# Kernel optimization log

Measured on AMD Instinct MI355X. Metric: run time of the kernel, lower is better.

## Reference

```python
import jax, jax.numpy as jnp
import numpy as np

N = 131072      # total nodes
E = 2097152     # total edges (~16 avg degree)
G = 1024        # number of graphs for mean pooling
NODE_DIM, EDGE_DIM, HID, OUT = 16, 6, 64, 128


def _lin(key, i, o):
    return jax.random.normal(key, (i, o), jnp.float32) * (1.0 / np.sqrt(i))


def setup_inputs() -> dict:
    key = jax.random.key(0)
    ks = jax.random.split(key, 12)
    return {
        "x": jax.random.normal(ks[0], (N, NODE_DIM), jnp.float32),
        "edge_attr": jax.random.normal(ks[1], (E, EDGE_DIM), jnp.float32),
        "edge_index": jax.random.randint(ks[2], (2, E), 0, N, jnp.int32),
        "batch": jnp.sort(jax.random.randint(ks[3], (N,), 0, G, jnp.int32)),
        # edge_mlp1: 2*16+6 -> 64 -> 64
        "w11": _lin(ks[4], 2 * NODE_DIM + EDGE_DIM, 64), "b11": jnp.zeros((64,), jnp.float32),
        "w12": _lin(ks[5], 64, HID), "b12": jnp.zeros((HID,), jnp.float32),
        # edge_mlp2: 2*64+6 -> 64 -> 64
        "w21": _lin(ks[6], 2 * HID + EDGE_DIM, 64), "b21": jnp.zeros((64,), jnp.float32),
        "w22": _lin(ks[7], 64, HID), "b22": jnp.zeros((HID,), jnp.float32),
        # readout: 64 -> 64 -> 128
        "wr1": _lin(ks[8], HID, 64), "br1": jnp.zeros((64,), jnp.float32),
        "wr2": _lin(ks[9], 64, OUT), "br2": jnp.zeros((OUT,), jnp.float32),
    }


def _edge_conv(h, edge_attr, src, dst, w1, b1, w2, b2):
    # PyG EdgeConv(aggr='max'): x_i = h[dst], x_j = h[src], scatter-max onto dst
    m = jnp.concatenate([h[dst], h[src], edge_attr], axis=-1)   # [E, 2D+edge_dim]
    m = jax.nn.relu(m @ w1 + b1) @ w2 + b2                       # [E, HID]
    agg = jax.ops.segment_max(m, dst, num_segments=h.shape[0])   # [N, HID]
    return jnp.where(jnp.isfinite(agg), agg, jnp.zeros_like(agg))  # empty nodes -> 0


def reference(x, edge_attr, edge_index, batch,
              w11, b11, w12, b12, w21, b21, w22, b22, wr1, br1, wr2, br2):
    src, dst = edge_index[0], edge_index[1]
    h = jax.nn.relu(_edge_conv(x, edge_attr, src, dst, w11, b11, w12, b12))
    h = jax.nn.relu(_edge_conv(h, edge_attr, src, dst, w21, b21, w22, b22))
    # global_mean_pool over batch ids
    sums = jax.ops.segment_sum(h, batch, num_segments=G)                       # [G, HID]
    cnts = jax.ops.segment_sum(jnp.ones((h.shape[0], 1), h.dtype), batch, num_segments=G)
    pooled = sums / jnp.maximum(cnts, 1.0)
    z = jax.nn.relu(pooled @ wr1 + br1) @ wr2 + br2                            # [G, OUT]
    return z
```

## Files before the change

### kernel.cpp

```cpp
#include <hip/hip_runtime.h>
#include <stdint.h>

#define NN 131072
#define NE 2097152
#define NG 1024

__device__ __forceinline__ unsigned enc_f32(float f) {
  unsigned b = __float_as_uint(f);
  return (b & 0x80000000u) ? ~b : (b | 0x80000000u);
}
__device__ __forceinline__ float dec_pos(unsigned u) {
  return __uint_as_float(u & 0x7fffffffu);
}

__global__ void init_ws(uint4* __restrict__ h1, uint4* __restrict__ h2,
                        int* __restrict__ counts, int* __restrict__ fill,
                        int* __restrict__ bcnt) {
  const int HN4 = NN * 64 / 4;
  uint4 v = make_uint4(0x80000000u, 0x80000000u, 0x80000000u, 0x80000000u);
  int stride = gridDim.x * blockDim.x;
  for (int t = blockIdx.x * blockDim.x + threadIdx.x; t < HN4; t += stride) {
    h1[t] = v;
    h2[t] = v;
  }
  for (int t = blockIdx.x * blockDim.x + threadIdx.x; t < NN; t += stride) {
    counts[t] = 0;
    fill[t] = 0;
  }
  for (int t = blockIdx.x * blockDim.x + threadIdx.x; t < NG; t += stride)
    bcnt[t] = 0;
}

__global__ __launch_bounds__(256) void count_all(const int* __restrict__ dst,
                                                 const int* __restrict__ batch,
                                                 int* __restrict__ counts,
                                                 int* __restrict__ bcnt) {
  int e = blockIdx.x * 256 + threadIdx.x;
  atomicAdd(&counts[dst[e]], 1);
  if (e < NN) atomicAdd(&bcnt[batch[e]], 1);
}

__global__ __launch_bounds__(256) void scanA(const int* __restrict__ counts,
                                             int* __restrict__ rp,
                                             int* __restrict__ bsum) {
  __shared__ int sm[256];
  int t = threadIdx.x;
  int g = blockIdx.x * 256 + t;
  int v = counts[g];
  sm[t] = v;
  __syncthreads();
  for (int off = 1; off < 256; off <<= 1) {
    int a = (t >= off) ? sm[t - off] : 0;
    __syncthreads();
    sm[t] += a;
    __syncthreads();
  }
  rp[g] = sm[t] - v;
  if (t == 255) bsum[blockIdx.x] = sm[255];
}

__global__ __launch_bounds__(512) void scanB(int* __restrict__ bsum) {
  __shared__ int sm[512];
  int t = threadIdx.x;
  int v = bsum[t];
  sm[t] = v;
  __syncthreads();
  for (int off = 1; off < 512; off <<= 1) {
    int a = (t >= off) ? sm[t - off] : 0;
    __syncthreads();
    sm[t] += a;
    __syncthreads();
  }
  bsum[t] = sm[t] - v;
}

__global__ __launch_bounds__(256) void scanC(int* __restrict__ rp,
                                             const int* __restrict__ bsum) {
  int g = blockIdx.x * 256 + threadIdx.x;
  rp[g] += bsum[blockIdx.x];
  if (g == 0) rp[NN] = NE;
}

__global__ __launch_bounds__(1024) void scan_batch(const int* __restrict__ bcnt,
                                                   int* __restrict__ bp) {
  __shared__ int sm[1024];
  int t = threadIdx.x;
  int v = bcnt[t];
  sm[t] = v;
  __syncthreads();
  for (int off = 1; off < 1024; off <<= 1) {
    int a = (t >= off) ? sm[t - off] : 0;
    __syncthreads();
    sm[t] += a;
    __syncthreads();
  }
  bp[t] = sm[t] - v;
  if (t == 1023) bp[NG] = NN;
}

__global__ __launch_bounds__(256) void scatter(
    const int* __restrict__ src, const int* __restrict__ dst,
    const float* __restrict__ ea, const int* __restrict__ rp,
    int* __restrict__ fill, int* __restrict__ eperm, int* __restrict__ sp,
    int* __restrict__ dst_p, float* __restrict__ ea_p, int use_eap) {
  int e = blockIdx.x * 256 + threadIdx.x;
  int d = dst[e];
  int p = rp[d] + atomicAdd(&fill[d], 1);
  sp[p] = src[e];
  dst_p[p] = d;
  if (use_eap) {
    const float2* s2 = (const float2*)(ea + (size_t)e * 6);
    float2 a = s2[0], b = s2[1], c = s2[2];
    float2* d2 = (float2*)(ea_p + (size_t)p * 6);
    d2[0] = a; d2[1] = b; d2[2] = c;
  } else {
    eperm[p] = e;
  }
}

__global__ __launch_bounds__(256, 4) void nodePQ1(
    const float* __restrict__ x, const float* __restrict__ w1,
    const float* __restrict__ b1, float* __restrict__ P, float* __restrict__ Q) {
  int half = blockIdx.x >> 9;
  int n = (blockIdx.x & 511) * 256 + threadIdx.x;
  const float* w = w1 + half * 16 * 64;
  float acc[64];
#pragma unroll
  for (int j = 0; j < 64; j++) acc[j] = half ? 0.0f : b1[j];
  const float4* x4 = (const float4*)(x + (size_t)n * 16);
#pragma unroll
  for (int kk = 0; kk < 4; kk++) {
    float4 v = x4[kk];
    const float* wr = w + (kk * 4) * 64;
#pragma unroll
    for (int j = 0; j < 64; j++) acc[j] = fmaf(v.x, wr[j], acc[j]);
#pragma unroll
    for (int j = 0; j < 64; j++) acc[j] = fmaf(v.y, wr[64 + j], acc[j]);
#pragma unroll
    for (int j = 0; j < 64; j++) acc[j] = fmaf(v.z, wr[128 + j], acc[j]);
#pragma unroll
    for (int j = 0; j < 64; j++) acc[j] = fmaf(v.w, wr[192 + j], acc[j]);
  }
  float4* o = (float4*)((half ? Q : P) + (size_t)n * 64);
#pragma unroll
  for (int j = 0; j < 16; j++)
    o[j] = make_float4(acc[4 * j], acc[4 * j + 1], acc[4 * j + 2], acc[4 * j + 3]);
}

__global__ __launch_bounds__(256, 4) void nodePQ2(
    const unsigned* __restrict__ h1, const float* __restrict__ w1,
    const float* __restrict__ b1, float* __restrict__ P, float* __restrict__ Q) {
  int half = blockIdx.x >> 9;
  int n = (blockIdx.x & 511) * 256 + threadIdx.x;
  const float* w = w1 + half * 64 * 64;
  float acc[64];
#pragma unroll
  for (int j = 0; j < 64; j++) acc[j] = half ? 0.0f : b1[j];
  const uint4* h4 = (const uint4*)(h1 + (size_t)n * 64);
#pragma unroll 4
  for (int kk = 0; kk < 16; kk++) {
    uint4 u = h4[kk];
    float v0 = dec_pos(u.x), v1 = dec_pos(u.y), v2 = dec_pos(u.z), v3 = dec_pos(u.w);
    const float* wr = w + (kk * 4) * 64;
#pragma unroll
    for (int j = 0; j < 64; j++) acc[j] = fmaf(v0, wr[j], acc[j]);
#pragma unroll
    for (int j = 0; j < 64; j++) acc[j] = fmaf(v1, wr[64 + j], acc[j]);
#pragma unroll
    for (int j = 0; j < 64; j++) acc[j] = fmaf(v2, wr[128 + j], acc[j]);
#pragma unroll
    for (int j = 0; j < 64; j++) acc[j] = fmaf(v3, wr[192 + j], acc[j]);
  }
  float4* o = (float4*)((half ? Q : P) + (size_t)n * 64);
#pragma unroll
  for (int j = 0; j < 16; j++)
    o[j] = make_float4(acc[4 * j], acc[4 * j + 1], acc[4 * j + 2], acc[4 * j + 3]);
}

template <bool EAP>
__global__ __launch_bounds__(256, 4) void edge_mlp(
    const float* __restrict__ P, const float* __restrict__ Q,
    const float* __restrict__ ea_p, const float* __restrict__ ea,
    const int* __restrict__ eperm, const int* __restrict__ sp,
    const int* __restrict__ dst_p, const int* __restrict__ rp,
    const float* __restrict__ w1c, const float* __restrict__ w2,
    const float* __restrict__ b2, unsigned* __restrict__ hout) {
  __shared__ float tile[4][64 * 32];
  __shared__ int dar[4][64];

  int tid = threadIdx.x;
  int wv = tid >> 6, lane = tid & 63;
  int g = blockIdx.x * 256 + tid;
  int wavebase = g - lane;
  int d = dst_p[g], s = sp[g];
  int seg_lo = rp[d], seg_hi = rp[d + 1];
  bool whole = (seg_lo >= wavebase) && (seg_hi <= wavebase + 64);
  dar[wv][lane] = d | (whole ? (int)0x80000000 : 0);

  float2 ev[3];
  if (EAP) {
    const float2* q = (const float2*)(ea_p + (size_t)g * 6);
    ev[0] = q[0]; ev[1] = q[1]; ev[2] = q[2];
  } else {
    int e = eperm[g];
    const float2* q = (const float2*)(ea + (size_t)e * 6);
    ev[0] = q[0]; ev[1] = q[1]; ev[2] = q[2];
  }

  const float4* Pd = (const float4*)(P + (size_t)d * 64);
  const float4* Qs = (const float4*)(Q + (size_t)s * 64);
  float* mytile = tile[wv];
  int swz = (lane & 7) << 2;

#pragma unroll 1
  for (int half = 0; half < 2; ++half) {
    float out[32];
#pragma unroll
    for (int o = 0; o < 32; o++) out[o] = b2[half * 32 + o];

#pragma unroll 1
    for (int jc = 0; jc < 4; ++jc) {
      float hj[16];
#pragma unroll
      for (int kk = 0; kk < 4; kk++) {
        float4 a = Pd[jc * 4 + kk];
        float4 b = Qs[jc * 4 + kk];
        hj[4 * kk]     = a.x + b.x;
        hj[4 * kk + 1] = a.y + b.y;
        hj[4 * kk + 2] = a.z + b.z;
        hj[4 * kk + 3] = a.w + b.w;
      }
#pragma unroll
      for (int t = 0; t < 3; t++) {
        const float* wr = w1c + (2 * t) * 64 + jc * 16;
#pragma unroll
        for (int j = 0; j < 16; j++) hj[j] = fmaf(ev[t].x, wr[j], hj[j]);
#pragma unroll
        for (int j = 0; j < 16; j++) hj[j] = fmaf(ev[t].y, wr[64 + j], hj[j]);
      }
#pragma unroll
      for (int j = 0; j < 16; j++) hj[j] = fmaxf(hj[j], 0.0f);

#pragma unroll
      for (int j = 0; j < 16; j++) {
        float hv = hj[j];
        const float* w2r = w2 + (jc * 16 + j) * 64 + half * 32;
#pragma unroll
        for (int o = 0; o < 32; o++) out[o] = fmaf(hv, w2r[o], out[o]);
      }
    }

#pragma unroll
    for (int k = 0; k < 8; ++k) {
      int cdst = (4 * k) ^ swz;
      *(float4*)&mytile[lane * 32 + cdst] =
          make_float4(out[4 * k], out[4 * k + 1], out[4 * k + 2], out[4 * k + 3]);
    }
    asm volatile("s_waitcnt lgkmcnt(0)" ::: "memory");

    if (lane < 32) {
      float mx = 0.0f;
      int cur = dar[wv][0];
#pragma unroll 8
      for (int e = 0; e < 64; ++e) {
        float v = mytile[e * 32 + (lane ^ ((e & 7) << 2))];
        mx = fmaxf(mx, v);
        int nxt = (e < 63) ? dar[wv][e + 1] : 0x7fffffff;
        if (cur != nxt) {
          unsigned encv = enc_f32(mx);
          unsigned* addr =
              hout + (size_t)(cur & 0x7fffffff) * 64 + half * 32 + lane;
          if (cur < 0) *addr = encv;
          else atomicMax(addr, encv);
          mx = 0.0f;
        }
        cur = nxt;
      }
    }
    asm volatile("s_waitcnt lgkmcnt(0)" ::: "memory");
  }
}

__global__ __launch_bounds__(256) void readout(
    const unsigned* __restrict__ h2, const int* __restrict__ bp,
    const float* __restrict__ wr1, const float* __restrict__ br1,
    const float* __restrict__ wr2, const float* __restrict__ br2,
    float* __restrict__ out) {
  int g = blockIdx.x;
  int tid = threadIdx.x;
  int wv = tid >> 6, lane = tid & 63;
  int lo = bp[g], hi = bp[g + 1];
  float s = 0.0f;
  for (int n = lo + wv; n < hi; n += 4) s += dec_pos(h2[(size_t)n * 64 + lane]);
  __shared__ float part[4][64];
  __shared__ float p[64], t[64];
  part[wv][lane] = s;
  __syncthreads();
  if (tid < 64) {
    float c = fmaxf((float)(hi - lo), 1.0f);
    p[tid] = (part[0][tid] + part[1][tid] + part[2][tid] + part[3][tid]) / c;
  }
  __syncthreads();
  if (tid < 64) {
    float a = br1[tid];
#pragma unroll 8
    for (int k = 0; k < 64; k++) a = fmaf(p[k], wr1[k * 64 + tid], a);
    t[tid] = fmaxf(a, 0.0f);
  }
  __syncthreads();
  if (tid < 64) {
    float z0 = br2[tid], z1 = br2[64 + tid];
#pragma unroll 8
    for (int k = 0; k < 64; k++) {
      float tk = t[k];
      z0 = fmaf(tk, wr2[k * 128 + tid], z0);
      z1 = fmaf(tk, wr2[k * 128 + 64 + tid], z1);
    }
    out[(size_t)g * 128 + tid] = z0;
    out[(size_t)g * 128 + 64 + tid] = z1;
  }
}

extern "C" void kernel_launch(void* const* d_in, const int* in_sizes, int n_in,
                              void* d_out, int out_size, void* d_ws, size_t ws_size,
                              hipStream_t stream) {
  const float* x     = (const float*)d_in[0];
  const float* ea    = (const float*)d_in[1];
  const int*   ei    = (const int*)d_in[2];
  const int*   batch = (const int*)d_in[3];
  const float* w11 = (const float*)d_in[4];
  const float* b11 = (const float*)d_in[5];
  const float* w12 = (const float*)d_in[6];
  const float* b12 = (const float*)d_in[7];
  const float* w21 = (const float*)d_in[8];
  const float* b21 = (const float*)d_in[9];
  const float* w22 = (const float*)d_in[10];
  const float* b22 = (const float*)d_in[11];
  const float* wr1 = (const float*)d_in[12];
  const float* br1 = (const float*)d_in[13];
  const float* wr2 = (const float*)d_in[14];
  const float* br2 = (const float*)d_in[15];
  float* out = (float*)d_out;

  const int* src = ei;
  const int* dst = ei + NE;

  char* ws = (char*)d_ws;
  size_t off = 0;
  auto alloc = [&](size_t bytes) {
    char* p = ws + off;
    off = (off + bytes + 255) & ~(size_t)255;
    return p;
  };
  unsigned* h1   = (unsigned*)alloc((size_t)NN * 64 * 4);
  unsigned* h2   = (unsigned*)alloc((size_t)NN * 64 * 4);
  float*    Pbuf = (float*)alloc((size_t)NN * 64 * 4);
  float*    Qbuf = (float*)alloc((size_t)NN * 64 * 4);
  int*   sp    = (int*)alloc((size_t)NE * 4);
  int*   eperm = (int*)alloc((size_t)NE * 4);
  int*   dst_p = (int*)alloc((size_t)NE * 4);
  int*   rp    = (int*)alloc((size_t)(NN + 1) * 4);
  int*   counts= (int*)alloc((size_t)NN * 4);
  int*   fill  = (int*)alloc((size_t)NN * 4);
  int*   bcnt  = (int*)alloc((size_t)NG * 4);
  int*   bp    = (int*)alloc((size_t)(NG + 1) * 4);
  int*   bsum  = (int*)alloc(512 * 4);
  float* ea_p  = (float*)alloc((size_t)NE * 6 * 4);
  int use_eap = (off <= ws_size) ? 1 : 0;

  init_ws<<<1024, 256, 0, stream>>>((uint4*)h1, (uint4*)h2, counts, fill, bcnt);
  count_all<<<NE / 256, 256, 0, stream>>>(dst, batch, counts, bcnt);
  scanA<<<NN / 256, 256, 0, stream>>>(counts, rp, bsum);
  scanB<<<1, 512, 0, stream>>>(bsum);
  scanC<<<NN / 256, 256, 0, stream>>>(rp, bsum);
  scan_batch<<<1, 1024, 0, stream>>>(bcnt, bp);
  scatter<<<NE / 256, 256, 0, stream>>>(src, dst, ea, rp, fill, eperm, sp,
                                        dst_p, ea_p, use_eap);

  nodePQ1<<<1024, 256, 0, stream>>>(x, w11, b11, Pbuf, Qbuf);
  if (use_eap)
    edge_mlp<true><<<NE / 256, 256, 0, stream>>>(Pbuf, Qbuf, ea_p, ea, eperm, sp,
                                                 dst_p, rp, w11 + 32 * 64, w12, b12, h1);
  else
    edge_mlp<false><<<NE / 256, 256, 0, stream>>>(Pbuf, Qbuf, ea_p, ea, eperm, sp,
                                                  dst_p, rp, w11 + 32 * 64, w12, b12, h1);

  nodePQ2<<<1024, 256, 0, stream>>>(h1, w21, b21, Pbuf, Qbuf);
  if (use_eap)
    edge_mlp<true><<<NE / 256, 256, 0, stream>>>(Pbuf, Qbuf, ea_p, ea, eperm, sp,
                                                 dst_p, rp, w21 + 128 * 64, w22, b22, h2);
  else
    edge_mlp<false><<<NE / 256, 256, 0, stream>>>(Pbuf, Qbuf, ea_p, ea, eperm, sp,
                                                  dst_p, rp, w21 + 128 * 64, w22, b22, h2);

  readout<<<NG, 256, 0, stream>>>(h2, bp, wr1, br1, wr2, br2, out);
}
```

Baseline: 1.214 ms.

## Use split-bf16 MFMA for the edge MLP second layer

Replaces the per-thread scalar FMA second-layer matmul in the edge MLP with 16x16x32 bf16 MFMA instructions. Activations and weights are split into bf16 hi and lo parts and combined with three MFMAs to approximate fp32 accuracy. A small prep kernel pre-packs the second-layer weights into the MFMA operand layout. Results are staged in a swizzled LDS tile for the existing segment-max atomics. The aim is to offload the dominant 64x64 FMA work per edge to matrix cores, at the cost of extra LDS traffic, packing overhead and slightly reduced precision.

```diff
diff --git a/kernel.cpp b/kernel.cpp
--- a/kernel.cpp
+++ b/kernel.cpp
@@ -5,12 +5,18 @@
 #define NE 2097152
 #define NG 1024
 
+typedef float f32x4 __attribute__((ext_vector_type(4)));
+typedef short bf16x8 __attribute__((ext_vector_type(8)));
+
 __device__ __forceinline__ unsigned enc_f32(float f) {
   unsigned b = __float_as_uint(f);
   return (b & 0x80000000u) ? ~b : (b | 0x80000000u);
 }
 __device__ __forceinline__ float dec_pos(unsigned u) {
   return __uint_as_float(u & 0x7fffffffu);
+}
+__device__ __forceinline__ unsigned pack_hi(unsigned u0, unsigned u1) {
+  return __builtin_amdgcn_perm(u1, u0, 0x07060302u);
 }
 
 __global__ void init_ws(uint4* __restrict__ h1, uint4* __restrict__ h2,
@@ -118,6 +124,33 @@
   }
 }
 
+__global__ __launch_bounds__(1024) void prep_w2(const float* __restrict__ w2a,
+                                                const float* __restrict__ w2b,
+                                                unsigned* __restrict__ w2f) {
+  int tid = threadIdx.x;
+  const float* w2 = blockIdx.x ? w2b : w2a;
+  unsigned* outp = w2f + blockIdx.x * 4096;
+  int dt = tid >> 9, kc = (tid >> 8) & 1, nt = (tid >> 6) & 3, lane = tid & 63;
+  int kbase = kc * 32 + (lane >> 4) * 8;
+  int n = nt * 16 + (lane & 15);
+  unsigned dwords[4];
+#pragma unroll
+  for (int i = 0; i < 4; i++) {
+    float w0 = w2[(kbase + 2 * i) * 64 + n];
+    float w1 = w2[(kbase + 2 * i + 1) * 64 + n];
+    unsigned u0 = __float_as_uint(w0), u1 = __float_as_uint(w1);
+    if (dt == 0) {
+      dwords[i] = pack_hi(u0, u1);
+    } else {
+      float l0 = w0 - __uint_as_float(u0 & 0xffff0000u);
+      float l1 = w1 - __uint_as_float(u1 & 0xffff0000u);
+      dwords[i] = pack_hi(__float_as_uint(l0), __float_as_uint(l1));
+    }
+  }
+  *(uint4*)(outp + ((dt * 2 + kc) * 4 + nt) * 256 + lane * 4) =
+      make_uint4(dwords[0], dwords[1], dwords[2], dwords[3]);
+}
+
 __global__ __launch_bounds__(256, 4) void nodePQ1(
     const float* __restrict__ x, const float* __restrict__ w1,
     const float* __restrict__ b1, float* __restrict__ P, float* __restrict__ Q) {
@@ -178,22 +211,22 @@
 }
 
 template <bool EAP>
-__global__ __launch_bounds__(256, 4) void edge_mlp(
+__global__ __launch_bounds__(256, 4) void edge_mfma(
     const float* __restrict__ P, const float* __restrict__ Q,
     const float* __restrict__ ea_p, const float* __restrict__ ea,
     const int* __restrict__ eperm, const int* __restrict__ sp,
     const int* __restrict__ dst_p, const int* __restrict__ rp,
-    const float* __restrict__ w1c, const float* __restrict__ w2,
+    const float* __restrict__ w1c, const unsigned* __restrict__ w2f,
     const float* __restrict__ b2, unsigned* __restrict__ hout) {
-  __shared__ float tile[4][64 * 32];
+  __shared__ __align__(16) unsigned lds[4][2176];
   __shared__ int dar[4][64];
 
-  int tid = threadIdx.x;
-  int wv = tid >> 6, lane = tid & 63;
+  int tid = threadIdx.x, wv = tid >> 6, lane = tid & 63;
+  int lc = lane & 15, lg = lane >> 4;
   int g = blockIdx.x * 256 + tid;
-  int wavebase = g - lane;
   int d = dst_p[g], s = sp[g];
   int seg_lo = rp[d], seg_hi = rp[d + 1];
+  int wavebase = g - lane;
   bool whole = (seg_lo >= wavebase) && (seg_hi <= wavebase + 64);
   dar[wv][lane] = d | (whole ? (int)0x80000000 : 0);
 
@@ -207,69 +240,114 @@
     ev[0] = q[0]; ev[1] = q[1]; ev[2] = q[2];
   }
 
-  const float4* Pd = (const float4*)(P + (size_t)d * 64);
-  const float4* Qs = (const float4*)(Q + (size_t)s * 64);
-  float* mytile = tile[wv];
-  int swz = (lane & 7) << 2;
-
+  f32x4 acc[4][4];
+#pragma unroll
+  for (int nt = 0; nt < 4; nt++) {
+    float bv = b2[nt * 16 + lc];
+#pragma unroll
+    for (int mt = 0; mt < 4; mt++) acc[mt][nt] = (f32x4){bv, bv, bv, bv};
+  }
+
+  unsigned* hi_t = lds[wv];
+  unsigned* lo_t = lds[wv] + 1024;
+  int kw = (lane >> 1) & 3;
+  int ka = (lc >> 1) & 3;
+
+#pragma unroll 1
+  for (int kc = 0; kc < 2; ++kc) {
+    float hj[32];
+    {
+      const float4* Pd = (const float4*)(P + (size_t)d * 64 + kc * 32);
+      const float4* Qs = (const float4*)(Q + (size_t)s * 64 + kc * 32);
+#pragma unroll
+      for (int i = 0; i < 8; i++) {
+        float4 a = Pd[i];
+        float4 b = Qs[i];
+        hj[4 * i] = a.x + b.x;
+        hj[4 * i + 1] = a.y + b.y;
+        hj[4 * i + 2] = a.z + b.z;
+        hj[4 * i + 3] = a.w + b.w;
+      }
+#pragma unroll
+      for (int t = 0; t < 3; t++) {
+        const float* wr = w1c + (2 * t) * 64 + kc * 32;
+#pragma unroll
+        for (int j = 0; j < 32; j++) hj[j] = fmaf(ev[t].x, wr[j], hj[j]);
+#pragma unroll
+        for (int j = 0; j < 32; j++) hj[j] = fmaf(ev[t].y, wr[64 + j], hj[j]);
+      }
+#pragma unroll
+      for (int j = 0; j < 32; j++) hj[j] = fmaxf(hj[j], 0.0f);
+    }
+
+    if (kc) asm volatile("s_waitcnt lgkmcnt(0)" ::: "memory");
+#pragma unroll
+    for (int q = 0; q < 4; q++) {
+      unsigned hd[4], ld_[4];
+#pragma unroll
+      for (int i = 0; i < 4; i++) {
+        float h0 = hj[q * 8 + 2 * i], h1 = hj[q * 8 + 2 * i + 1];
+        unsigned u0 = __float_as_uint(h0), u1 = __float_as_uint(h1);
+        hd[i] = pack_hi(u0, u1);
+        float l0 = h0 - __uint_as_float(u0 & 0xffff0000u);
+        float l1 = h1 - __uint_as_float(u1 & 0xffff0000u);
+        ld_[i] = pack_hi(__float_as_uint(l0), __float_as_uint(l1));
+      }
+      int a = lane * 16 + 4 * (q ^ kw);
+      *(uint4*)(hi_t + a) = make_uint4(hd[0], hd[1], hd[2], hd[3]);
+      *(uint4*)(lo_t + a) = make_uint4(ld_[0], ld_[1], ld_[2], ld_[3]);
+    }
+    asm volatile("s_waitcnt lgkmcnt(0)" ::: "memory");
+
+    bf16x8 ah[4], al[4];
+#pragma unroll
+    for (int mt = 0; mt < 4; mt++) {
+      int a = (mt * 16 + lc) * 16 + 4 * (lg ^ ka);
+      ah[mt] = *(bf16x8*)(hi_t + a);
+      al[mt] = *(bf16x8*)(lo_t + a);
+    }
+#pragma unroll
+    for (int nt = 0; nt < 4; nt++) {
+      bf16x8 bh = *(const bf16x8*)(w2f + ((0 + kc) * 4 + nt) * 256 + lane * 4);
+      bf16x8 bl = *(const bf16x8*)(w2f + ((2 + kc) * 4 + nt) * 256 + lane * 4);
+#pragma unroll
+      for (int mt = 0; mt < 4; mt++) {
+        acc[mt][nt] = __builtin_amdgcn_mfma_f32_16x16x32_bf16(ah[mt], bh, acc[mt][nt], 0, 0, 0);
+        acc[mt][nt] = __builtin_amdgcn_mfma_f32_16x16x32_bf16(ah[mt], bl, acc[mt][nt], 0, 0, 0);
+        acc[mt][nt] = __builtin_amdgcn_mfma_f32_16x16x32_bf16(al[mt], bh, acc[mt][nt], 0, 0, 0);
+      }
+    }
+  }
+
+  float* ct = (float*)lds[wv];
+  int kx = 4 * ((lane >> 3) & 3);
 #pragma unroll 1
   for (int half = 0; half < 2; ++half) {
-    float out[32];
-#pragma unroll
-    for (int o = 0; o < 32; o++) out[o] = b2[half * 32 + o];
-
-#pragma unroll 1
-    for (int jc = 0; jc < 4; ++jc) {
-      float hj[16];
-#pragma unroll
-      for (int kk = 0; kk < 4; kk++) {
-        float4 a = Pd[jc * 4 + kk];
-        float4 b = Qs[jc * 4 + kk];
-        hj[4 * kk]     = a.x + b.x;
-        hj[4 * kk + 1] = a.y + b.y;
-        hj[4 * kk + 2] = a.z + b.z;
-        hj[4 * kk + 3] = a.w + b.w;
-      }
-#pragma unroll
-      for (int t = 0; t < 3; t++) {
-        const float* wr = w1c + (2 * t) * 64 + jc * 16;
-#pragma unroll
-        for (int j = 0; j < 16; j++) hj[j] = fmaf(ev[t].x, wr[j], hj[j]);
-#pragma unroll
-        for (int j = 0; j < 16; j++) hj[j] = fmaf(ev[t].y, wr[64 + j], hj[j]);
-      }
-#pragma unroll
-      for (int j = 0; j < 16; j++) hj[j] = fmaxf(hj[j], 0.0f);
-
-#pragma unroll
-      for (int j = 0; j < 16; j++) {
-        float hv = hj[j];
-        const float* w2r = w2 + (jc * 16 + j) * 64 + half * 32;
-#pragma unroll
-        for (int o = 0; o < 32; o++) out[o] = fmaf(hv, w2r[o], out[o]);
-      }
-    }
-
-#pragma unroll
-    for (int k = 0; k < 8; ++k) {
-      int cdst = (4 * k) ^ swz;
-      *(float4*)&mytile[lane * 32 + cdst] =
-          make_float4(out[4 * k], out[4 * k + 1], out[4 * k + 2], out[4 * k + 3]);
-    }
     asm volatile("s_waitcnt lgkmcnt(0)" ::: "memory");
-
+#pragma unroll
+    for (int nt2 = 0; nt2 < 2; nt2++) {
+      int nt = half * 2 + nt2;
+      int chl = nt2 * 16 + lc;
+      int kc2 = 4 * ((chl >> 3) & 3);
+#pragma unroll
+      for (int mt = 0; mt < 4; mt++) {
+        int cb = (mt * 16 + 4 * lg) ^ kc2;
+        *(f32x4*)(ct + chl * 68 + cb) = acc[mt][nt];
+      }
+    }
+    asm volatile("s_waitcnt lgkmcnt(0)" ::: "memory");
     if (lane < 32) {
       float mx = 0.0f;
       int cur = dar[wv][0];
+      int base = lane * 68;
 #pragma unroll 8
       for (int e = 0; e < 64; ++e) {
-        float v = mytile[e * 32 + (lane ^ ((e & 7) << 2))];
+        float v = ct[base + (e ^ kx)];
         mx = fmaxf(mx, v);
         int nxt = (e < 63) ? dar[wv][e + 1] : 0x7fffffff;
         if (cur != nxt) {
+          unsigned* addr = hout + (size_t)(cur & 0x7fffffff) * 64 + half * 32 + lane;
           unsigned encv = enc_f32(mx);
-          unsigned* addr =
-              hout + (size_t)(cur & 0x7fffffff) * 64 + half * 32 + lane;
           if (cur < 0) *addr = encv;
           else atomicMax(addr, encv);
           mx = 0.0f;
@@ -277,7 +355,6 @@
         cur = nxt;
       }
     }
-    asm volatile("s_waitcnt lgkmcnt(0)" ::: "memory");
   }
 }
 
@@ -365,6 +442,7 @@
   int*   bcnt  = (int*)alloc((size_t)NG * 4);
   int*   bp    = (int*)alloc((size_t)(NG + 1) * 4);
   int*   bsum  = (int*)alloc(512 * 4);
+  unsigned* w2f = (unsigned*)alloc(2 * 4096 * 4);
   float* ea_p  = (float*)alloc((size_t)NE * 6 * 4);
   int use_eap = (off <= ws_size) ? 1 : 0;
 
@@ -376,22 +454,23 @@
   scan_batch<<<1, 1024, 0, stream>>>(bcnt, bp);
   scatter<<<NE / 256, 256, 0, stream>>>(src, dst, ea, rp, fill, eperm, sp,
                                         dst_p, ea_p, use_eap);
+  prep_w2<<<2, 1024, 0, stream>>>(w12, w22, w2f);
 
   nodePQ1<<<1024, 256, 0, stream>>>(x, w11, b11, Pbuf, Qbuf);
   if (use_eap)
-    edge_mlp<true><<<NE / 256, 256, 0, stream>>>(Pbuf, Qbuf, ea_p, ea, eperm, sp,
-                                                 dst_p, rp, w11 + 32 * 64, w12, b12, h1);
+    edge_mfma<true><<<NE / 256, 256, 0, stream>>>(Pbuf, Qbuf, ea_p, ea, eperm, sp,
+                                                  dst_p, rp, w11 + 32 * 64, w2f, b12, h1);
   else
-    edge_mlp<false><<<NE / 256, 256, 0, stream>>>(Pbuf, Qbuf, ea_p, ea, eperm, sp,
-                                                  dst_p, rp, w11 + 32 * 64, w12, b12, h1);
+    edge_mfma<false><<<NE / 256, 256, 0, stream>>>(Pbuf, Qbuf, ea_p, ea, eperm, sp,
+                                                   dst_p, rp, w11 + 32 * 64, w2f, b12, h1);
 
   nodePQ2<<<1024, 256, 0, stream>>>(h1, w21, b21, Pbuf, Qbuf);
   if (use_eap)
-    edge_mlp<true><<<NE / 256, 256, 0, stream>>>(Pbuf, Qbuf, ea_p, ea, eperm, sp,
-                                                 dst_p, rp, w21 + 128 * 64, w22, b22, h2);
+    edge_mfma<true><<<NE / 256, 256, 0, stream>>>(Pbuf, Qbuf, ea_p, ea, eperm, sp,
+                                                  dst_p, rp, w21 + 128 * 64, w2f + 4096, b22, h2);
   else
-    edge_mlp<false><<<NE / 256, 256, 0, stream>>>(Pbuf, Qbuf, ea_p, ea, eperm, sp,
-                                                  dst_p, rp, w21 + 128 * 64, w22, b22, h2);
+    edge_mfma<false><<<NE / 256, 256, 0, stream>>>(Pbuf, Qbuf, ea_p, ea, eperm, sp,
+                                                   dst_p, rp, w21 + 128 * 64, w2f + 4096, b22, h2);
 
   readout<<<NG, 256, 0, stream>>>(h2, bp, wr1, br1, wr2, br2, out);
 }
```

After: 1.870 ms. 54.1% more time.
